# Kernel optimization log

Hardware: AMD Instinct MI355X
Metric: run time of the kernel (lower is better)

The kernel has to match this reference:

```python
import jax, jax.numpy as jnp
import numpy as np

NB = 8  # num_blocks

def setup_inputs() -> dict:
    key = jax.random.key(0)
    ks = jax.random.split(key, 8)
    C = 128
    C8 = C // 8
    s = 0.05
    x = jax.random.normal(ks[0], (1, C, 64, 64, 64), dtype=jnp.float32)
    Wq = jax.random.normal(ks[1], (C8, C), dtype=jnp.float32) * s
    bq = jax.random.normal(ks[2], (C8,), dtype=jnp.float32) * s
    Wk = jax.random.normal(ks[3], (C8, C), dtype=jnp.float32) * s
    bk = jax.random.normal(ks[4], (C8,), dtype=jnp.float32) * s
    Wv = jax.random.normal(ks[5], (C, C), dtype=jnp.float32) * s
    bv = jax.random.normal(ks[6], (C,), dtype=jnp.float32) * s
    # torch inits gamma=0 (output == x, zero grads through attention);
    # use 0.5 so the attention path is actually exercised.
    gamma = jnp.full((1,), 0.5, dtype=jnp.float32)
    return dict(x=x, Wq=Wq, bq=bq, Wk=Wk, bk=bk, Wv=Wv, bv=bv, gamma=gamma)

def reference(x, Wq, bq, Wk, bk, Wv, bv, gamma):
    B, C, D, H, W = x.shape
    db, hb, wb = D // NB, H // NB, W // NB
    n = db * hb * wb
    # (i, j, k, B, C, db, hb, wb) block layout
    xr = x.reshape(B, C, NB, db, NB, hb, NB, wb).transpose(2, 4, 6, 0, 1, 3, 5, 7)
    ar = jnp.arange(NB)
    # NOTE: original code computes k = i % num_blocks, i.e. k == i always.
    # Only the (i, j, i) diagonal blocks are attended; the rest stay zero in `out`.
    blk = xr[ar, :, ar].reshape(NB * NB * B, C, n)  # (P, C, n), P = NB*NB*B
    # 1x1x1 convs == per-voxel linear layers over channels
    q = jnp.einsum('pcn,dc->pdn', blk, Wq) + bq[None, :, None]  # (P, C/8, n)
    k = jnp.einsum('pcn,dc->pdn', blk, Wk) + bk[None, :, None]  # (P, C/8, n)
    v = jnp.einsum('pcn,dc->pdn', blk, Wv) + bv[None, :, None]  # (P, C,   n)
    attn = jax.nn.softmax(jnp.einsum('pdn,pdm->pnm', q, k), axis=-1)  # (P, n_q, n_k)
    ob = jnp.einsum('pdm,pnm->pdn', v, attn)  # value @ attn^T, (P, C, n)
    ob = ob.reshape(NB, NB, B, C, db, hb, wb)
    out = jnp.zeros_like(xr).at[ar, :, ar].set(ob)  # only k==i diagonal filled
    out = out.transpose(3, 4, 0, 5, 1, 6, 2, 7).reshape(B, C, D, H, W)
    return gamma * out + x
```

## Files before the change

### kernel.cpp

```cpp
#include <hip/hip_runtime.h>

typedef __attribute__((ext_vector_type(8))) short bf16x8;
typedef __attribute__((ext_vector_type(4))) float f32x4;
typedef __attribute__((ext_vector_type(4))) int i32x4;
typedef __attribute__((ext_vector_type(4))) float float4v;

#define MFMA16(a, b, c) __builtin_amdgcn_mfma_f32_16x16x32_bf16((a), (b), (c), 0, 0, 0)

__device__ __forceinline__ unsigned short f2bf(float f) {
    unsigned u = __builtin_bit_cast(unsigned, f);
    u += 0x7fffu + ((u >> 16) & 1u);
    return (unsigned short)(u >> 16);
}
__device__ __forceinline__ float bf2f(unsigned short s) {
    unsigned u = ((unsigned)s) << 16;
    return __builtin_bit_cast(float, u);
}
__device__ __forceinline__ int pkbf(float a, float b) {
    return (int)f2bf(a) | ((int)f2bf(b) << 16);
}

#define KOFF 131072
#define LOFF 147456

__global__ __launch_bounds__(1024, 1) void battn_kernel(
    const float* __restrict__ x,
    const float* __restrict__ Wq, const float* __restrict__ bq,
    const float* __restrict__ Wk, const float* __restrict__ bk,
    const float* __restrict__ Wv, const float* __restrict__ bv,
    const float* __restrict__ gamma, float* __restrict__ out)
{
    __shared__ __attribute__((aligned(128))) char smem[147968];
    const int tid = threadIdx.x;
    const int bid = blockIdx.x;
    const int p  = ((bid & 7) << 3) | (bid >> 5);
    const int qq = (bid >> 3) & 3;
    const int ib = p >> 3, jb = p & 7;
    const int vbase = ib * 8 * 4096 + jb * 8 * 64 + ib * 8;
    const int lane = tid & 63, wv = tid >> 6;
    const int g = lane >> 4, c15 = lane & 15;
    const f32x4 zacc = {0.f, 0.f, 0.f, 0.f};
    const bf16x8 zfrag = (bf16x8)(short)0;

    #pragma unroll
    for (int b = 0; b < 2; ++b) {
        float4v t[8];
        #pragma unroll
        for (int j = 0; j < 8; ++j) {
            int ch = (b * 8 + j) * 1024 + tid;
            int c = ch >> 7;
            int m = (ch & 127) * 4;
            int vox = ((m >> 6) << 12) + (((m >> 3) & 7) << 6) + (m & 7);
            t[j] = *(const float4v*)(x + c * 262144 + vbase + vox);
        }
        #pragma unroll
        for (int j = 0; j < 8; ++j) {
            int ch = (b * 8 + j) * 1024 + tid;
            int c = ch >> 7;
            int m = (ch & 127) * 4;
            char* bp = smem + ((m * 256 + 2 * c) ^ (((m >> 2) & 7) << 4));
            *(unsigned short*)(bp)       = f2bf(t[j][0]);
            *(unsigned short*)(bp + 256) = f2bf(t[j][1]);
            *(unsigned short*)(bp + 512) = f2bf(t[j][2]);
            *(unsigned short*)(bp + 768) = f2bf(t[j][3]);
        }
    }

    bf16x8 wqf[4], wkf[4], wvf[4];
    float bqv = 0.f, bkv = 0.f;
    if (wv < 8) {
        #pragma unroll
        for (int ks = 0; ks < 4; ++ks) {
            const float4v* sq = (const float4v*)(Wq + c15 * 128 + ks * 32 + g * 8);
            const float4v* sk = (const float4v*)(Wk + c15 * 128 + ks * 32 + g * 8);
            const float4v* sv = (const float4v*)(Wv + (wv * 16 + c15) * 128 + ks * 32 + g * 8);
            float4v q0 = sq[0], q1 = sq[1];
            float4v k0 = sk[0], k1 = sk[1];
            float4v v0 = sv[0], v1 = sv[1];
            #pragma unroll
            for (int e = 0; e < 4; ++e) {
                wqf[ks][e] = (short)f2bf(q0[e]); wqf[ks][4 + e] = (short)f2bf(q1[e]);
                wkf[ks][e] = (short)f2bf(k0[e]); wkf[ks][4 + e] = (short)f2bf(k1[e]);
                wvf[ks][e] = (short)f2bf(v0[e]); wvf[ks][4 + e] = (short)f2bf(v1[e]);
            }
        }
        bqv = bq[c15]; bkv = bk[c15];
    }

    __syncthreads();

    bf16x8 qf = zfrag;
    if (wv < 8) {
        {
            f32x4 acc = zacc;
            int mrow = qq * 128 + wv * 16 + c15;
            int sw = ((mrow >> 2) & 7) << 4;
            #pragma unroll
            for (int ks = 0; ks < 4; ++ks) {
                bf16x8 af = *(const bf16x8*)(smem + ((mrow * 256 + ks * 64 + g * 16) ^ sw));
                acc = MFMA16(af, wqf[ks], acc);
            }
            #pragma unroll
            for (int r = 0; r < 4; ++r)
                *(unsigned short*)(smem + KOFF + wv * 2048 + (g * 4 + r) * 32 + 2 * c15) = f2bf(acc[r] + bqv);
        }
        if (g < 2) qf = *(const bf16x8*)(smem + KOFF + wv * 2048 + c15 * 32 + g * 16);

        #pragma unroll
        for (int qi = 0; qi < 4; ++qi) {
            f32x4 acc = zacc;
            int mrow = wv * 64 + qi * 16 + c15;
            int sw = ((mrow >> 2) & 7) << 4;
            #pragma unroll
            for (int ks = 0; ks < 4; ++ks) {
                bf16x8 af = *(const bf16x8*)(smem + ((mrow * 256 + ks * 64 + g * 16) ^ sw));
                acc = MFMA16(af, wkf[ks], acc);
            }
            #pragma unroll
            for (int r = 0; r < 4; ++r) {
                int mk = wv * 64 + qi * 16 + g * 4 + r;
                *(unsigned short*)(smem + KOFF + mk * 32 + 2 * c15) = f2bf(acc[r] + bkv);
            }
        }
    }

    for (int ck = 0; ck < 4; ++ck) {
        f32x4 vacc[8];
        if (wv < 8) {
            #pragma unroll
            for (int mt = 0; mt < 8; ++mt) {
                vacc[mt] = zacc;
                int mrow = ck * 128 + mt * 16 + c15;
                int sw = ((mrow >> 2) & 7) << 4;
                #pragma unroll
                for (int ks = 0; ks < 4; ++ks) {
                    bf16x8 bf = *(const bf16x8*)(smem + ((mrow * 256 + ks * 64 + g * 16) ^ sw));
                    vacc[mt] = MFMA16(wvf[ks], bf, vacc[mt]);
                }
            }
        }
        __syncthreads();
        if (wv < 8) {
            #pragma unroll
            for (int mt = 0; mt < 8; ++mt) {
                #pragma unroll
                for (int r = 0; r < 4; ++r) {
                    int c_out = wv * 16 + g * 4 + r;
                    int mkl = mt * 16 + c15;
                    *(unsigned short*)(smem + ck * 32768 + c_out * 256 +
                                       ((2 * mkl) ^ ((c_out & 7) << 4))) = f2bf(vacc[mt][r]);
                }
            }
        }
    }
    __syncthreads();

    float xv[32];
    int go_e = 0;
    float invl_dummy;
    (void)invl_dummy;
    if (wv >= 8) {
        int t = tid - 512;
        int q128 = t & 127;
        int cb = t >> 7;
        int nq = qq * 128 + q128;
        int vox = ((nq >> 6) << 12) + (((nq >> 3) & 7) << 6) + (nq & 7);
        go_e = vbase + vox;
        #pragma unroll
        for (int i = 0; i < 32; ++i) {
            int c = cb * 32 + i;
            xv[i] = out[c * 262144 + go_e];
        }
    }

    if (wv < 8) {
        f32x4 o[8];
        #pragma unroll
        for (int ci = 0; ci < 8; ++ci) o[ci] = zacc;
        float lsum = 0.f;

        for (int kt = 0; kt < 16; ++kt) {
            int mk0 = kt * 32;
            bf16x8 ka[2];
            #pragma unroll
            for (int ki = 0; ki < 2; ++ki) {
                bf16x8 v = zfrag;
                if (g < 2) v = *(const bf16x8*)(smem + KOFF + (mk0 + ki * 16 + c15) * 32 + g * 16);
                ka[ki] = v;
            }

            f32x4 s0 = MFMA16(ka[0], qf, zacc);
            f32x4 s1 = MFMA16(ka[1], qf, zacc);
            float e00 = __expf(s0[0]), e01 = __expf(s0[1]), e02 = __expf(s0[2]), e03 = __expf(s0[3]);
            float e10 = __expf(s1[0]), e11 = __expf(s1[1]), e12 = __expf(s1[2]), e13 = __expf(s1[3]);
            lsum += (e00 + e01) + (e02 + e03) + ((e10 + e11) + (e12 + e13));
            int wA0 = pkbf(e00, e01), wB0 = pkbf(e02, e03);
            int wA1 = pkbf(e10, e11), wB1 = pkbf(e12, e13);
            int src1 = ((2 * g) & 3) * 16 + c15;
            int src2 = ((2 * g + 1) & 3) * 16 + c15;
            int sA0a = __shfl(wA0, src1, 64), sA1a = __shfl(wA1, src1, 64);
            int sB0a = __shfl(wB0, src1, 64), sB1a = __shfl(wB1, src1, 64);
            int sA0b = __shfl(wA0, src2, 64), sA1b = __shfl(wA1, src2, 64);
            int sB0b = __shfl(wB0, src2, 64), sB1b = __shfl(wB1, src2, 64);
            bool k1 = (g >= 2);
            i32x4 uu = { k1 ? sA1a : sA0a, k1 ? sB1a : sB0a,
                         k1 ? sA1b : sA0b, k1 ? sB1b : sB0b };
            bf16x8 pa = __builtin_bit_cast(bf16x8, uu);

            int ckbase = (mk0 >> 7) * 32768;
            int mklb = (2 * (mk0 & 127)) + 16 * g;
            #pragma unroll
            for (int ci = 0; ci < 8; ++ci) {
                int c = ci * 16 + c15;
                bf16x8 vb = *(const bf16x8*)(smem + ckbase + c * 256 + (mklb ^ ((c & 7) << 4)));
                o[ci] = MFMA16(pa, vb, o[ci]);
            }
        }

        {
            float l = lsum;
            l += __shfl_xor(l, 16, 64);
            l += __shfl_xor(l, 32, 64);
            if (g == 0)
                *(float*)(smem + LOFF + (wv * 16 + c15) * 4) = l;
        }

        __syncthreads();

        #pragma unroll
        for (int ci = 0; ci < 8; ++ci)
            #pragma unroll
            for (int r = 0; r < 4; ++r) {
                int nql = wv * 16 + g * 4 + r;
                int c = ci * 16 + c15;
                *(unsigned short*)(smem + c * 256 + ((2 * nql) ^ ((c & 7) << 4))) = f2bf(o[ci][r]);
            }
        __syncthreads();
    } else {
        __syncthreads();
        __syncthreads();
    }

    if (wv >= 8) {
        float gma = gamma[0];
        int t = tid - 512;
        int q128 = t & 127;
        int cb = t >> 7;
        float invl = 1.0f / *(const float*)(smem + LOFF + q128 * 4);
        #pragma unroll
        for (int i = 0; i < 32; ++i) {
            int c = cb * 32 + i;
            float ov = bf2f(*(const unsigned short*)(smem + c * 256 + ((2 * q128) ^ ((c & 7) << 4))));
            out[c * 262144 + go_e] = gma * (ov * invl + bv[c]) + xv[i];
        }
    }
}

extern "C" void kernel_launch(void* const* d_in, const int* in_sizes, int n_in,
                              void* d_out, int out_size, void* d_ws, size_t ws_size,
                              hipStream_t stream) {
    const float* x     = (const float*)d_in[0];
    const float* Wq    = (const float*)d_in[1];
    const float* bq    = (const float*)d_in[2];
    const float* Wk    = (const float*)d_in[3];
    const float* bk    = (const float*)d_in[4];
    const float* Wv    = (const float*)d_in[5];
    const float* bv    = (const float*)d_in[6];
    const float* gamma = (const float*)d_in[7];
    float* out = (float*)d_out;
    (void)in_sizes; (void)n_in; (void)out_size; (void)d_ws; (void)ws_size;

    hipMemcpyAsync(out, x, (size_t)out_size * sizeof(float),
                   hipMemcpyDeviceToDevice, stream);
    battn_kernel<<<dim3(256), dim3(1024), 0, stream>>>(x, Wq, bq, Wk, bk, Wv, bv, gamma, out);
}
```

Before: 93.13 us.

## Spread V projection and epilogue across all waves; vectorize x staging; pad K rows

The V projection work, previously done by 8 of 16 waves across four serial chunks with a barrier each, is now split so every wave computes two chunks, which drops three barriers. The epilogue and the x prefetch are likewise spread over all 1024 threads instead of half. The initial x-to-LDS staging now packs eight channels into one 16-byte store instead of scalar 2-byte stores. The Q/K row stride goes from 32 to 40 bytes to reduce LDS bank conflicts, which grows shared memory slightly and raises register pressure in the V stage.

New measurement: 97.98 us. 1.05x slower.

```diff
diff --git a/kernel.cpp b/kernel.cpp
--- a/kernel.cpp
+++ b/kernel.cpp
@@ -21,7 +21,7 @@
 }
 
 #define KOFF 131072
-#define LOFF 147456
+#define LOFF 151552
 
 __global__ __launch_bounds__(1024, 1) void battn_kernel(
     const float* __restrict__ x,
@@ -30,62 +30,70 @@
     const float* __restrict__ Wv, const float* __restrict__ bv,
     const float* __restrict__ gamma, float* __restrict__ out)
 {
-    __shared__ __attribute__((aligned(128))) char smem[147968];
+    __shared__ __attribute__((aligned(128))) char smem[152064];
     const int tid = threadIdx.x;
     const int bid = blockIdx.x;
     const int p  = ((bid & 7) << 3) | (bid >> 5);
     const int qq = (bid >> 3) & 3;
     const int ib = p >> 3, jb = p & 7;
-    const int vbase = ib * 8 * 4096 + jb * 8 * 64 + ib * 8;
+    const int vbase = ib * 32768 + jb * 512 + ib * 8;
     const int lane = tid & 63, wv = tid >> 6;
     const int g = lane >> 4, c15 = lane & 15;
     const f32x4 zacc = {0.f, 0.f, 0.f, 0.f};
     const bf16x8 zfrag = (bf16x8)(short)0;
 
-    #pragma unroll
-    for (int b = 0; b < 2; ++b) {
-        float4v t[8];
-        #pragma unroll
-        for (int j = 0; j < 8; ++j) {
-            int ch = (b * 8 + j) * 1024 + tid;
-            int c = ch >> 7;
-            int m = (ch & 127) * 4;
-            int vox = ((m >> 6) << 12) + (((m >> 3) & 7) << 6) + (m & 7);
-            t[j] = *(const float4v*)(x + c * 262144 + vbase + vox);
-        }
-        #pragma unroll
-        for (int j = 0; j < 8; ++j) {
-            int ch = (b * 8 + j) * 1024 + tid;
-            int c = ch >> 7;
-            int m = (ch & 127) * 4;
-            char* bp = smem + ((m * 256 + 2 * c) ^ (((m >> 2) & 7) << 4));
-            *(unsigned short*)(bp)       = f2bf(t[j][0]);
-            *(unsigned short*)(bp + 256) = f2bf(t[j][1]);
-            *(unsigned short*)(bp + 512) = f2bf(t[j][2]);
-            *(unsigned short*)(bp + 768) = f2bf(t[j][3]);
+    {
+        int pi0 = tid, pi1 = tid + 1024;
+        int c0a = (pi0 & 15) * 8, m0a = (pi0 >> 4) * 4;
+        int c0b = (pi1 & 15) * 8, m0b = (pi1 >> 4) * 4;
+        int voxa = ((m0a >> 6) << 12) + (((m0a >> 3) & 7) << 6) + (m0a & 7);
+        int voxb = ((m0b >> 6) << 12) + (((m0b >> 3) & 7) << 6) + (m0b & 7);
+        float4v t0[8], t1[8];
+        #pragma unroll
+        for (int j = 0; j < 8; ++j)
+            t0[j] = *(const float4v*)(x + (c0a + j) * 262144 + vbase + voxa);
+        #pragma unroll
+        for (int j = 0; j < 8; ++j)
+            t1[j] = *(const float4v*)(x + (c0b + j) * 262144 + vbase + voxb);
+        #pragma unroll
+        for (int r = 0; r < 4; ++r) {
+            int m = m0a + r;
+            i32x4 w = { pkbf(t0[0][r], t0[1][r]), pkbf(t0[2][r], t0[3][r]),
+                        pkbf(t0[4][r], t0[5][r]), pkbf(t0[6][r], t0[7][r]) };
+            *(i32x4*)(smem + ((m * 256 + 2 * c0a) ^ (((m >> 2) & 7) << 4))) = w;
+        }
+        #pragma unroll
+        for (int r = 0; r < 4; ++r) {
+            int m = m0b + r;
+            i32x4 w = { pkbf(t1[0][r], t1[1][r]), pkbf(t1[2][r], t1[3][r]),
+                        pkbf(t1[4][r], t1[5][r]), pkbf(t1[6][r], t1[7][r]) };
+            *(i32x4*)(smem + ((m * 256 + 2 * c0b) ^ (((m >> 2) & 7) << 4))) = w;
         }
     }
 
     bf16x8 wqf[4], wkf[4], wvf[4];
     float bqv = 0.f, bkv = 0.f;
-    if (wv < 8) {
-        #pragma unroll
-        for (int ks = 0; ks < 4; ++ks) {
+    #pragma unroll
+    for (int ks = 0; ks < 4; ++ks) {
+        const float4v* sv = (const float4v*)(Wv + ((wv & 7) * 16 + c15) * 128 + ks * 32 + g * 8);
+        float4v v0 = sv[0], v1 = sv[1];
+        #pragma unroll
+        for (int e = 0; e < 4; ++e) {
+            wvf[ks][e] = (short)f2bf(v0[e]); wvf[ks][4 + e] = (short)f2bf(v1[e]);
+        }
+        if (wv < 8) {
             const float4v* sq = (const float4v*)(Wq + c15 * 128 + ks * 32 + g * 8);
             const float4v* sk = (const float4v*)(Wk + c15 * 128 + ks * 32 + g * 8);
-            const float4v* sv = (const float4v*)(Wv + (wv * 16 + c15) * 128 + ks * 32 + g * 8);
             float4v q0 = sq[0], q1 = sq[1];
             float4v k0 = sk[0], k1 = sk[1];
-            float4v v0 = sv[0], v1 = sv[1];
             #pragma unroll
             for (int e = 0; e < 4; ++e) {
                 wqf[ks][e] = (short)f2bf(q0[e]); wqf[ks][4 + e] = (short)f2bf(q1[e]);
                 wkf[ks][e] = (short)f2bf(k0[e]); wkf[ks][4 + e] = (short)f2bf(k1[e]);
-                wvf[ks][e] = (short)f2bf(v0[e]); wvf[ks][4 + e] = (short)f2bf(v1[e]);
-            }
-        }
-        bqv = bq[c15]; bkv = bk[c15];
-    }
+            }
+        }
+    }
+    if (wv < 8) { bqv = bq[c15]; bkv = bk[c15]; }
 
     __syncthreads();
 
@@ -102,9 +110,9 @@
             }
             #pragma unroll
             for (int r = 0; r < 4; ++r)
-                *(unsigned short*)(smem + KOFF + wv * 2048 + (g * 4 + r) * 32 + 2 * c15) = f2bf(acc[r] + bqv);
-        }
-        if (g < 2) qf = *(const bf16x8*)(smem + KOFF + wv * 2048 + c15 * 32 + g * 16);
+                *(unsigned short*)(smem + KOFF + wv * 2560 + (g * 4 + r) * 40 + 2 * c15) = f2bf(acc[r] + bqv);
+        }
+        if (g < 2) qf = *(const bf16x8*)(smem + KOFF + wv * 2560 + c15 * 40 + g * 16);
 
         #pragma unroll
         for (int qi = 0; qi < 4; ++qi) {
@@ -119,58 +127,53 @@
             #pragma unroll
             for (int r = 0; r < 4; ++r) {
                 int mk = wv * 64 + qi * 16 + g * 4 + r;
-                *(unsigned short*)(smem + KOFF + mk * 32 + 2 * c15) = f2bf(acc[r] + bkv);
-            }
-        }
-    }
-
-    for (int ck = 0; ck < 4; ++ck) {
-        f32x4 vacc[8];
-        if (wv < 8) {
+                *(unsigned short*)(smem + KOFF + mk * 40 + 2 * c15) = f2bf(acc[r] + bkv);
+            }
+        }
+    }
+
+    {
+        const int ck0 = (wv >> 3) * 2;
+        f32x4 vacc[2][8];
+        #pragma unroll
+        for (int cc = 0; cc < 2; ++cc)
             #pragma unroll
             for (int mt = 0; mt < 8; ++mt) {
-                vacc[mt] = zacc;
-                int mrow = ck * 128 + mt * 16 + c15;
+                vacc[cc][mt] = zacc;
+                int mrow = (ck0 + cc) * 128 + mt * 16 + c15;
                 int sw = ((mrow >> 2) & 7) << 4;
                 #pragma unroll
                 for (int ks = 0; ks < 4; ++ks) {
                     bf16x8 bf = *(const bf16x8*)(smem + ((mrow * 256 + ks * 64 + g * 16) ^ sw));
-                    vacc[mt] = MFMA16(wvf[ks], bf, vacc[mt]);
+                    vacc[cc][mt] = MFMA16(wvf[ks], bf, vacc[cc][mt]);
                 }
             }
-        }
-        __syncthreads();
-        if (wv < 8) {
-            #pragma unroll
-            for (int mt = 0; mt < 8; ++mt) {
+        __syncthreads();
+        #pragma unroll
+        for (int cc = 0; cc < 2; ++cc)
+            #pragma unroll
+            for (int mt = 0; mt < 8; ++mt)
                 #pragma unroll
                 for (int r = 0; r < 4; ++r) {
-                    int c_out = wv * 16 + g * 4 + r;
+                    int c_out = (wv & 7) * 16 + g * 4 + r;
                     int mkl = mt * 16 + c15;
-                    *(unsigned short*)(smem + ck * 32768 + c_out * 256 +
-                                       ((2 * mkl) ^ ((c_out & 7) << 4))) = f2bf(vacc[mt][r]);
+                    *(unsigned short*)(smem + (ck0 + cc) * 32768 + c_out * 256 +
+                                       ((2 * mkl) ^ ((c_out & 7) << 4))) = f2bf(vacc[cc][mt][r]);
                 }
-            }
-        }
     }
     __syncthreads();
 
-    float xv[32];
-    int go_e = 0;
-    float invl_dummy;
-    (void)invl_dummy;
-    if (wv >= 8) {
-        int t = tid - 512;
-        int q128 = t & 127;
-        int cb = t >> 7;
-        int nq = qq * 128 + q128;
-        int vox = ((nq >> 6) << 12) + (((nq >> 3) & 7) << 6) + (nq & 7);
-        go_e = vbase + vox;
-        #pragma unroll
-        for (int i = 0; i < 32; ++i) {
-            int c = cb * 32 + i;
-            xv[i] = out[c * 262144 + go_e];
-        }
+    const int q128 = tid & 127;
+    const int h8 = tid >> 7;
+    float xv[16];
+    int go_e;
+    {
+        int nq_e = qq * 128 + q128;
+        int vox_e = ((nq_e >> 6) << 12) + (((nq_e >> 3) & 7) << 6) + (nq_e & 7);
+        go_e = vbase + vox_e;
+        #pragma unroll
+        for (int i = 0; i < 16; ++i)
+            xv[i] = out[(h8 * 16 + i) * 262144 + go_e];
     }
 
     if (wv < 8) {
@@ -185,7 +188,7 @@
             #pragma unroll
             for (int ki = 0; ki < 2; ++ki) {
                 bf16x8 v = zfrag;
-                if (g < 2) v = *(const bf16x8*)(smem + KOFF + (mk0 + ki * 16 + c15) * 32 + g * 16);
+                if (g < 2) v = *(const bf16x8*)(smem + KOFF + (mk0 + ki * 16 + c15) * 40 + g * 16);
                 ka[ki] = v;
             }
 
@@ -241,15 +244,12 @@
         __syncthreads();
     }
 
-    if (wv >= 8) {
+    {
         float gma = gamma[0];
-        int t = tid - 512;
-        int q128 = t & 127;
-        int cb = t >> 7;
         float invl = 1.0f / *(const float*)(smem + LOFF + q128 * 4);
         #pragma unroll
-        for (int i = 0; i < 32; ++i) {
-            int c = cb * 32 + i;
+        for (int i = 0; i < 16; ++i) {
+            int c = h8 * 16 + i;
             float ov = bf2f(*(const unsigned short*)(smem + c * 256 + ((2 * q128) ^ ((c & 7) << 4))));
             out[c * 262144 + go_e] = gma * (ov * invl + bv[c]) + xv[i];
         }
```

## Specialize waves so V projection overlaps Q/K projection and attention

Applied to the files above, without the earlier changes.

Waves 8-15 used to sit idle during the projections. They now load Wv and compute the V projection in two halves. Meanwhile waves 0-7 compute Q/K and the first half of the score/exp tiles. The key loop is split at the midpoint, so the first half of P@V runs while waves 8-15 store the second V half, with extra barriers between phases. The cost is more registers (vacc[2][8], pa[8]) and a later residual load of x, which now overlaps less with compute.

Result: slower. 135.6 us (+45.6%).

```diff
diff --git a/kernel.cpp b/kernel.cpp
--- a/kernel.cpp
+++ b/kernel.cpp
@@ -36,7 +36,7 @@
     const int p  = ((bid & 7) << 3) | (bid >> 5);
     const int qq = (bid >> 3) & 3;
     const int ib = p >> 3, jb = p & 7;
-    const int vbase = ib * 8 * 4096 + jb * 8 * 64 + ib * 8;
+    const int vbase = ib * 32768 + jb * 512 + ib * 8;
     const int lane = tid & 63, wv = tid >> 6;
     const int g = lane >> 4, c15 = lane & 15;
     const f32x4 zacc = {0.f, 0.f, 0.f, 0.f};
@@ -73,23 +73,32 @@
         for (int ks = 0; ks < 4; ++ks) {
             const float4v* sq = (const float4v*)(Wq + c15 * 128 + ks * 32 + g * 8);
             const float4v* sk = (const float4v*)(Wk + c15 * 128 + ks * 32 + g * 8);
-            const float4v* sv = (const float4v*)(Wv + (wv * 16 + c15) * 128 + ks * 32 + g * 8);
             float4v q0 = sq[0], q1 = sq[1];
             float4v k0 = sk[0], k1 = sk[1];
-            float4v v0 = sv[0], v1 = sv[1];
             #pragma unroll
             for (int e = 0; e < 4; ++e) {
                 wqf[ks][e] = (short)f2bf(q0[e]); wqf[ks][4 + e] = (short)f2bf(q1[e]);
                 wkf[ks][e] = (short)f2bf(k0[e]); wkf[ks][4 + e] = (short)f2bf(k1[e]);
+            }
+        }
+        bqv = bq[c15]; bkv = bk[c15];
+    } else {
+        #pragma unroll
+        for (int ks = 0; ks < 4; ++ks) {
+            const float4v* sv = (const float4v*)(Wv + ((wv & 7) * 16 + c15) * 128 + ks * 32 + g * 8);
+            float4v v0 = sv[0], v1 = sv[1];
+            #pragma unroll
+            for (int e = 0; e < 4; ++e) {
                 wvf[ks][e] = (short)f2bf(v0[e]); wvf[ks][4 + e] = (short)f2bf(v1[e]);
             }
         }
-        bqv = bq[c15]; bkv = bk[c15];
     }
 
     __syncthreads();
 
     bf16x8 qf = zfrag;
+    f32x4 vacc[2][8];
+
     if (wv < 8) {
         {
             f32x4 acc = zacc;
@@ -122,64 +131,55 @@
                 *(unsigned short*)(smem + KOFF + mk * 32 + 2 * c15) = f2bf(acc[r] + bkv);
             }
         }
-    }
-
-    for (int ck = 0; ck < 4; ++ck) {
-        f32x4 vacc[8];
-        if (wv < 8) {
+    } else {
+        #pragma unroll
+        for (int cc = 0; cc < 2; ++cc)
             #pragma unroll
             for (int mt = 0; mt < 8; ++mt) {
-                vacc[mt] = zacc;
-                int mrow = ck * 128 + mt * 16 + c15;
+                vacc[cc][mt] = zacc;
+                int mrow = cc * 128 + mt * 16 + c15;
                 int sw = ((mrow >> 2) & 7) << 4;
                 #pragma unroll
                 for (int ks = 0; ks < 4; ++ks) {
                     bf16x8 bf = *(const bf16x8*)(smem + ((mrow * 256 + ks * 64 + g * 16) ^ sw));
-                    vacc[mt] = MFMA16(wvf[ks], bf, vacc[mt]);
+                    vacc[cc][mt] = MFMA16(wvf[ks], bf, vacc[cc][mt]);
                 }
             }
-        }
-        __syncthreads();
-        if (wv < 8) {
-            #pragma unroll
-            for (int mt = 0; mt < 8; ++mt) {
+    }
+
+    __syncthreads();
+
+    bf16x8 pa[8];
+    float lsum = 0.f;
+
+    if (wv >= 8) {
+        #pragma unroll
+        for (int cc = 0; cc < 2; ++cc)
+            #pragma unroll
+            for (int mt = 0; mt < 8; ++mt)
                 #pragma unroll
                 for (int r = 0; r < 4; ++r) {
-                    int c_out = wv * 16 + g * 4 + r;
+                    int c_out = (wv & 7) * 16 + g * 4 + r;
                     int mkl = mt * 16 + c15;
-                    *(unsigned short*)(smem + ck * 32768 + c_out * 256 +
-                                       ((2 * mkl) ^ ((c_out & 7) << 4))) = f2bf(vacc[mt][r]);
+                    *(unsigned short*)(smem + cc * 32768 + c_out * 256 +
+                                       ((2 * mkl) ^ ((c_out & 7) << 4))) = f2bf(vacc[cc][mt][r]);
                 }
-            }
-        }
-    }
-    __syncthreads();
-
-    float xv[32];
-    int go_e = 0;
-    float invl_dummy;
-    (void)invl_dummy;
-    if (wv >= 8) {
-        int t = tid - 512;
-        int q128 = t & 127;
-        int cb = t >> 7;
-        int nq = qq * 128 + q128;
-        int vox = ((nq >> 6) << 12) + (((nq >> 3) & 7) << 6) + (nq & 7);
-        go_e = vbase + vox;
-        #pragma unroll
-        for (int i = 0; i < 32; ++i) {
-            int c = cb * 32 + i;
-            xv[i] = out[c * 262144 + go_e];
-        }
-    }
-
-    if (wv < 8) {
-        f32x4 o[8];
-        #pragma unroll
-        for (int ci = 0; ci < 8; ++ci) o[ci] = zacc;
-        float lsum = 0.f;
-
-        for (int kt = 0; kt < 16; ++kt) {
+        #pragma unroll
+        for (int cc = 0; cc < 2; ++cc)
+            #pragma unroll
+            for (int mt = 0; mt < 8; ++mt) {
+                vacc[cc][mt] = zacc;
+                int mrow = (2 + cc) * 128 + mt * 16 + c15;
+                int sw = ((mrow >> 2) & 7) << 4;
+                #pragma unroll
+                for (int ks = 0; ks < 4; ++ks) {
+                    bf16x8 bf = *(const bf16x8*)(smem + ((mrow * 256 + ks * 64 + g * 16) ^ sw));
+                    vacc[cc][mt] = MFMA16(wvf[ks], bf, vacc[cc][mt]);
+                }
+            }
+    } else {
+        #pragma unroll
+        for (int kt = 0; kt < 8; ++kt) {
             int mk0 = kt * 32;
             bf16x8 ka[2];
             #pragma unroll
@@ -188,7 +188,6 @@
                 if (g < 2) v = *(const bf16x8*)(smem + KOFF + (mk0 + ki * 16 + c15) * 32 + g * 16);
                 ka[ki] = v;
             }
-
             f32x4 s0 = MFMA16(ka[0], qf, zacc);
             f32x4 s1 = MFMA16(ka[1], qf, zacc);
             float e00 = __expf(s0[0]), e01 = __expf(s0[1]), e02 = __expf(s0[2]), e03 = __expf(s0[3]);
@@ -205,15 +204,80 @@
             bool k1 = (g >= 2);
             i32x4 uu = { k1 ? sA1a : sA0a, k1 ? sB1a : sB0a,
                          k1 ? sA1b : sA0b, k1 ? sB1b : sB0b };
-            bf16x8 pa = __builtin_bit_cast(bf16x8, uu);
-
+            pa[kt] = __builtin_bit_cast(bf16x8, uu);
+        }
+    }
+
+    __syncthreads();
+
+    f32x4 o[8];
+    #pragma unroll
+    for (int ci = 0; ci < 8; ++ci) o[ci] = zacc;
+
+    if (wv >= 8) {
+        #pragma unroll
+        for (int cc = 0; cc < 2; ++cc)
+            #pragma unroll
+            for (int mt = 0; mt < 8; ++mt)
+                #pragma unroll
+                for (int r = 0; r < 4; ++r) {
+                    int c_out = (wv & 7) * 16 + g * 4 + r;
+                    int mkl = mt * 16 + c15;
+                    *(unsigned short*)(smem + (2 + cc) * 32768 + c_out * 256 +
+                                       ((2 * mkl) ^ ((c_out & 7) << 4))) = f2bf(vacc[cc][mt][r]);
+                }
+    } else {
+        #pragma unroll
+        for (int kt = 0; kt < 8; ++kt) {
+            int mk0 = kt * 32;
             int ckbase = (mk0 >> 7) * 32768;
             int mklb = (2 * (mk0 & 127)) + 16 * g;
             #pragma unroll
             for (int ci = 0; ci < 8; ++ci) {
                 int c = ci * 16 + c15;
                 bf16x8 vb = *(const bf16x8*)(smem + ckbase + c * 256 + (mklb ^ ((c & 7) << 4)));
-                o[ci] = MFMA16(pa, vb, o[ci]);
+                o[ci] = MFMA16(pa[kt], vb, o[ci]);
+            }
+        }
+    }
+
+    __syncthreads();
+
+    if (wv < 8) {
+        for (int kt = 8; kt < 16; ++kt) {
+            int mk0 = kt * 32;
+            bf16x8 ka[2];
+            #pragma unroll
+            for (int ki = 0; ki < 2; ++ki) {
+                bf16x8 v = zfrag;
+                if (g < 2) v = *(const bf16x8*)(smem + KOFF + (mk0 + ki * 16 + c15) * 32 + g * 16);
+                ka[ki] = v;
+            }
+            f32x4 s0 = MFMA16(ka[0], qf, zacc);
+            f32x4 s1 = MFMA16(ka[1], qf, zacc);
+            float e00 = __expf(s0[0]), e01 = __expf(s0[1]), e02 = __expf(s0[2]), e03 = __expf(s0[3]);
+            float e10 = __expf(s1[0]), e11 = __expf(s1[1]), e12 = __expf(s1[2]), e13 = __expf(s1[3]);
+            lsum += (e00 + e01) + (e02 + e03) + ((e10 + e11) + (e12 + e13));
+            int wA0 = pkbf(e00, e01), wB0 = pkbf(e02, e03);
+            int wA1 = pkbf(e10, e11), wB1 = pkbf(e12, e13);
+            int src1 = ((2 * g) & 3) * 16 + c15;
+            int src2 = ((2 * g + 1) & 3) * 16 + c15;
+            int sA0a = __shfl(wA0, src1, 64), sA1a = __shfl(wA1, src1, 64);
+            int sB0a = __shfl(wB0, src1, 64), sB1a = __shfl(wB1, src1, 64);
+            int sA0b = __shfl(wA0, src2, 64), sA1b = __shfl(wA1, src2, 64);
+            int sB0b = __shfl(wB0, src2, 64), sB1b = __shfl(wB1, src2, 64);
+            bool k1 = (g >= 2);
+            i32x4 uu = { k1 ? sA1a : sA0a, k1 ? sB1a : sB0a,
+                         k1 ? sA1b : sA0b, k1 ? sB1b : sB0b };
+            bf16x8 pb = __builtin_bit_cast(bf16x8, uu);
+
+            int ckbase = (mk0 >> 7) * 32768;
+            int mklb = (2 * (mk0 & 127)) + 16 * g;
+            #pragma unroll
+            for (int ci = 0; ci < 8; ++ci) {
+                int c = ci * 16 + c15;
+                bf16x8 vb = *(const bf16x8*)(smem + ckbase + c * 256 + (mklb ^ ((c & 7) << 4)));
+                o[ci] = MFMA16(pb, vb, o[ci]);
             }
         }
 
@@ -225,8 +289,6 @@
                 *(float*)(smem + LOFF + (wv * 16 + c15) * 4) = l;
         }
 
-        __syncthreads();
-
         #pragma unroll
         for (int ci = 0; ci < 8; ++ci)
             #pragma unroll
@@ -235,11 +297,25 @@
                 int c = ci * 16 + c15;
                 *(unsigned short*)(smem + c * 256 + ((2 * nql) ^ ((c & 7) << 4))) = f2bf(o[ci][r]);
             }
-        __syncthreads();
-    } else {
-        __syncthreads();
-        __syncthreads();
-    }
+    }
+
+    float xv[32];
+    int go_e = 0;
+    if (wv >= 8) {
+        int t = tid - 512;
+        int q128 = t & 127;
+        int cb = t >> 7;
+        int nq = qq * 128 + q128;
+        int vox = ((nq >> 6) << 12) + (((nq >> 3) & 7) << 6) + (nq & 7);
+        go_e = vbase + vox;
+        #pragma unroll
+        for (int i = 0; i < 32; ++i) {
+            int c = cb * 32 + i;
+            xv[i] = out[c * 262144 + go_e];
+        }
+    }
+
+    __syncthreads();
 
     if (wv >= 8) {
         float gma = gamma[0];
```
